# Optimization experiments

Hardware: AMD Instinct MI355X
Metric: run time of the kernel (lower is better)

The kernel has to match this reference:

```python
import jax, jax.numpy as jnp
import numpy as np

T = 16384       # tokens (flattened leading dims)
D_IN = 1024     # in_features
D_OUT = 1024    # out_features
E = 8           # n_models (experts)


def setup_inputs() -> dict:
    key = jax.random.key(0)
    kx, ki, kw, kb = jax.random.split(key, 4)
    x = jax.random.normal(kx, (T, D_IN), dtype=jnp.float32)
    idxs = jax.random.randint(ki, (T,), 0, E, dtype=jnp.int32)
    # Per-expert Linear params (nn.Linear default-ish init scale)
    scale = 1.0 / np.sqrt(D_IN)
    W = jax.random.uniform(kw, (E, D_IN, D_OUT), dtype=jnp.float32, minval=-scale, maxval=scale)
    b = jax.random.uniform(kb, (E, D_OUT), dtype=jnp.float32, minval=-scale, maxval=scale)
    return {"x": x, "idxs": idxs, "W": W, "b": b}


def reference(x, idxs, W, b):
    # Original: for each expert i, y[idxs==i] = Linear_i(x[idxs==i]); return relu(y).
    # Equivalent math: each token t gets expert idxs[t]'s linear.
    # Compute all experts densely (E is small), then gather the assigned row.
    ys = jnp.einsum('ti,eio->eto', x, W) + b[:, None, :]   # [E, T, D_OUT]
    y = ys[idxs, jnp.arange(x.shape[0])]                    # [T, D_OUT] pick assigned expert
    return jax.nn.relu(y)
```

## Files before the change

kernel.cpp:

```cpp
#include <hip/hip_runtime.h>
#include <hip/hip_bf16.h>
#include <stdint.h>


#define T_TOK 16384
#define DIN   1024
#define DOUT  1024
#define NE    8
#define BM    128
#define BN    128
#define BK    64
#define TPX   17
#define MAX_TILES 136
#define MP_MAX (T_TOK + NE * BM)

typedef __attribute__((ext_vector_type(8))) short short8;
typedef __attribute__((ext_vector_type(4))) short short4v;
typedef __attribute__((ext_vector_type(4))) float floatx4;
typedef __attribute__((ext_vector_type(4))) int int4v;

__device__ __forceinline__ short f2b(float f) {
  return __builtin_bit_cast(short, __float2bfloat16(f));
}
__device__ __forceinline__ float b2f(unsigned short u) {
  unsigned v = ((unsigned)u) << 16;
  return __builtin_bit_cast(float, v);
}
__device__ __forceinline__ void glds16(const void* g, void* l) {
  __builtin_amdgcn_global_load_lds(
      (__attribute__((address_space(1))) void*)g,
      (__attribute__((address_space(3))) void*)l, 16, 0, 0);
}

#define FLAG_OFF    0
#define NTILES_OFF  64
#define TABLE_OFF   1024
#define TPAD_OFF    8192
#define WT_OFF      81920
#define XB_OFF      16859136
#define WS_NEED     (16859136UL + (size_t)T_TOK * DIN * 2)

#define TRANS_BLOCKS 512
#define CONV_BLOCKS  1024

__global__ __launch_bounds__(1024) void k_front(
    const unsigned short* __restrict__ xu, const int* __restrict__ idxs,
    const void* __restrict__ Wsrc, short* __restrict__ Wt, short* __restrict__ xb,
    int* __restrict__ flag, int* __restrict__ ntiles,
    int4v* __restrict__ table, int* __restrict__ tpad) {
  __shared__ int fS;
  __shared__ unsigned short tile[128][130];
  __shared__ int wtot[16][NE], waveBase[16][NE];
  __shared__ int totS[NE], padS[NE + 1];

  int tid = threadIdx.x;
  if (tid == 0) fS = 0;
  __syncthreads();
  if (tid < 256) {
    int ex = (xu[tid] >> 7) & 0xFF;
    if (ex >= 0xC0) atomicOr(&fS, 1);
  }
  __syncthreads();
  int fp32 = fS;

  if (blockIdx.x >= 1 + TRANS_BLOCKS) {
    if (!fp32) return;
    int b2 = blockIdx.x - (1 + TRANS_BLOCKS);
    size_t base = ((size_t)b2 * 1024 + tid) * 16;
    const float* src = (const float*)xu + base;
    floatx4 a0 = *(const floatx4*)(src + 0);
    floatx4 a1 = *(const floatx4*)(src + 4);
    floatx4 a2 = *(const floatx4*)(src + 8);
    floatx4 a3 = *(const floatx4*)(src + 12);
    short8 o0, o1;
    #pragma unroll
    for (int j = 0; j < 4; ++j) {
      o0[j] = f2b(a0[j]); o0[4 + j] = f2b(a1[j]);
      o1[j] = f2b(a2[j]); o1[4 + j] = f2b(a3[j]);
    }
    *(short8*)(xb + base) = o0;
    *(short8*)(xb + base + 8) = o1;
    return;
  }

  if (blockIdx.x != 0) {
    int b = blockIdx.x - 1;
    int e = b >> 6, kt = (b >> 3) & 7, nt8 = b & 7;
    size_t ibase = (size_t)e * DIN * DOUT + (size_t)(kt * 128) * DOUT + nt8 * 128;
    int k = tid >> 3, n16 = (tid & 7) * 16;
    if (fp32) {
      const float* p = (const float*)Wsrc + ibase + (size_t)k * DOUT + n16;
      #pragma unroll
      for (int g = 0; g < 4; ++g) {
        floatx4 a = *(const floatx4*)(p + g * 4);
        #pragma unroll
        for (int j = 0; j < 4; ++j) tile[k][n16 + g * 4 + j] = (unsigned short)f2b(a[j]);
      }
    } else {
      const short* p = (const short*)Wsrc + ibase + (size_t)k * DOUT + n16;
      #pragma unroll
      for (int g = 0; g < 2; ++g) {
        short8 v = *(const short8*)(p + g * 8);
        #pragma unroll
        for (int j = 0; j < 8; ++j) tile[k][n16 + g * 8 + j] = (unsigned short)v[j];
      }
    }
    __syncthreads();
    int n = tid >> 3, k16 = (tid & 7) * 16;
    short8 o0, o1;
    #pragma unroll
    for (int j = 0; j < 8; ++j) {
      o0[j] = (short)tile[k16 + j][n];
      o1[j] = (short)tile[k16 + 8 + j][n];
    }
    size_t obase = (size_t)e * DOUT * DIN + (size_t)(nt8 * 128 + n) * DIN + kt * 128 + k16;
    *(short8*)(Wt + obase) = o0;
    *(short8*)(Wt + obase + 8) = o1;
    return;
  }

  int lane = tid & 63, w = tid >> 6;
  if (tid == 0) *flag = fp32;

  int c[NE];
  #pragma unroll
  for (int e = 0; e < NE; ++e) c[e] = 0;
  const int4v* iv = (const int4v*)idxs;
  int4v vv[4];
  #pragma unroll
  for (int it = 0; it < 4; ++it) {
    vv[it] = iv[tid * 4 + it];
    ++c[vv[it].x]; ++c[vv[it].y]; ++c[vv[it].z]; ++c[vv[it].w];
  }
  int incl[NE];
  #pragma unroll
  for (int e = 0; e < NE; ++e) {
    incl[e] = c[e];
    #pragma unroll
    for (int d = 1; d < 64; d <<= 1) {
      int o = __shfl_up(incl[e], d);
      if (lane >= d) incl[e] += o;
    }
  }
  if (lane == 63) {
    #pragma unroll
    for (int e = 0; e < NE; ++e) wtot[w][e] = incl[e];
  }
  __syncthreads();
  if (tid < NE) {
    int s = 0;
    for (int ww = 0; ww < 16; ++ww) s += wtot[ww][tid];
    totS[tid] = s;
  }
  __syncthreads();
  if (tid == 0) {
    int p = 0, tc = 0;
    for (int e = 0; e < NE; ++e) {
      padS[e] = p;
      int cn = totS[e];
      int nmt = (cn + BM - 1) >> 7;
      for (int m = 0; m < nmt; ++m) table[tc++] = (int4v){e, p + m * BM, 0, 0};
      p += nmt * BM;
    }
    padS[NE] = p;
    *ntiles = tc;
  }
  __syncthreads();
  if (tid < 128) {
    int ww = tid >> 3, e = tid & 7;
    int s = padS[e];
    for (int wp = 0; wp < ww; ++wp) s += wtot[wp][e];
    waveBase[ww][e] = s;
  }
  __syncthreads();
  int base[NE];
  #pragma unroll
  for (int e = 0; e < NE; ++e) base[e] = waveBase[w][e] + incl[e] - c[e];
  #pragma unroll
  for (int it = 0; it < 4; ++it) {
    #pragma unroll
    for (int cm = 0; cm < 4; ++cm) {
      int te = vv[it][cm];
      int tk = tid * 16 + it * 4 + cm;
      #pragma unroll
      for (int e0 = 0; e0 < NE; ++e0)
        if (te == e0) tpad[base[e0]++] = tk;
    }
  }
  #pragma unroll
  for (int e = 0; e < NE; ++e) {
    int start = padS[e] + totS[e];
    int len = padS[e + 1] - start;
    if (tid < len) tpad[start + tid] = -1;
  }
}

#define STAGE(bb, k0)                                                       \
  {                                                                         \
    _Pragma("unroll")                                                       \
    for (int s4 = 0; s4 < 4; ++s4)                                          \
      glds16(bG[s4] + (k0), (char*)lB[bb] + ldsOff[s4]);                    \
    _Pragma("unroll")                                                       \
    for (int s4 = 0; s4 < 4; ++s4)                                          \
      glds16(aG[s4] + (size_t)(k0) * 2, (char*)lA[bb] + ldsOff[s4]);        \
  }

__launch_bounds__(256, 2)
__global__ void k_gemm(const void* __restrict__ xv, const short* __restrict__ xb,
                       const void* __restrict__ bv,
                       const short* __restrict__ Wt, const int* __restrict__ tpad,
                       const int* __restrict__ ntilesp, const int4v* __restrict__ table,
                       const int* __restrict__ flagp, void* __restrict__ outv) {
  int bid = blockIdx.x;
  int xcd = bid & 7;
  int s = bid >> 3;
  int nt = s & 7;
  int ti = s >> 3;
  int t = xcd * TPX + ti;
  if (t >= *ntilesp) return;
  int4v te = table[t];
  int e = te.x, arow0 = te.y;
  int fp32 = *flagp;

  int tid = threadIdx.x;
  int lane = tid & 63;
  int wave = tid >> 6;

  __shared__ short lA[2][BM * BK];
  __shared__ short lB[2][BN * BK];
  __shared__ int tokS[BM];

  if (tid < BM) tokS[tid] = tpad[arow0 + tid];
  __syncthreads();

  const short* WtE = Wt + (size_t)e * DOUT * DIN + (size_t)(nt * BN) * DIN;
  const char* aBase = fp32 ? (const char*)xb : (const char*)xv;

  const char* aG[4];
  const short* bG[4];
  int ldsOff[4];
  #pragma unroll
  for (int s4 = 0; s4 < 4; ++s4) {
    int fl = tid + s4 * 256;
    int r = fl >> 3, p = fl & 7;
    int kc = p ^ (r & 7);
    int tok = tokS[r];
    if (tok < 0) tok = 0;
    aG[s4] = aBase + (size_t)tok * (DIN * 2) + kc * 16;
    bG[s4] = WtE + (size_t)r * DIN + kc * 8;
    ldsOff[s4] = (s4 * 256 + wave * 64) * 16;
  }

  int wm = wave & 1, wn = wave >> 1;
  int lrow = lane & 15, q = lane >> 4;
  int aOff[4][2], bOff[4][2];
  #pragma unroll
  for (int i = 0; i < 4; ++i) {
    int m = wm * 64 + i * 16 + lrow;
    #pragma unroll
    for (int h = 0; h < 2; ++h)
      aOff[i][h] = m * BK + (((h * 4 + q) ^ (m & 7)) * 8);
  }
  #pragma unroll
  for (int j = 0; j < 4; ++j) {
    int n = wn * 64 + j * 16 + lrow;
    #pragma unroll
    for (int h = 0; h < 2; ++h)
      bOff[j][h] = n * BK + (((h * 4 + q) ^ (n & 7)) * 8);
  }

  floatx4 acc[4][4];
  #pragma unroll
  for (int i = 0; i < 4; ++i)
    #pragma unroll
    for (int j = 0; j < 4; ++j)
      acc[i][j] = (floatx4){0.f, 0.f, 0.f, 0.f};

  STAGE(0, 0);
  asm volatile("s_waitcnt vmcnt(0)\n\ts_barrier" ::: "memory");

  int cur = 0;
  for (int kt = 0; kt < DIN / BK; ++kt) {
    if (kt < DIN / BK - 1) STAGE(cur ^ 1, (kt + 1) * BK);
    #pragma unroll
    for (int h = 0; h < 2; ++h) {
      short8 af[4], bf[4];
      #pragma unroll
      for (int i = 0; i < 4; ++i) af[i] = *(const short8*)(&lA[cur][0] + aOff[i][h]);
      #pragma unroll
      for (int j = 0; j < 4; ++j) bf[j] = *(const short8*)(&lB[cur][0] + bOff[j][h]);
      #pragma unroll
      for (int i = 0; i < 4; ++i)
        #pragma unroll
        for (int j = 0; j < 4; ++j)
          acc[i][j] = __builtin_amdgcn_mfma_f32_16x16x32_bf16(bf[j], af[i], acc[i][j], 0, 0, 0);
    }
    asm volatile("s_waitcnt vmcnt(0)\n\ts_barrier" ::: "memory");
    cur ^= 1;
  }

  #pragma unroll
  for (int i = 0; i < 4; ++i) {
    int tok = tokS[wm * 64 + i * 16 + lrow];
    if (tok < 0) continue;
    size_t rowb = (size_t)tok * DOUT + nt * BN + wn * 64 + q * 4;
    #pragma unroll
    for (int j = 0; j < 4; ++j) {
      int n = nt * BN + wn * 64 + j * 16 + q * 4;
      if (fp32) {
        floatx4 b4 = *(const floatx4*)((const float*)bv + e * DOUT + n);
        floatx4 o;
        #pragma unroll
        for (int r = 0; r < 4; ++r) {
          float v = acc[i][j][r] + b4[r];
          o[r] = v > 0.f ? v : 0.f;
        }
        *(floatx4*)((float*)outv + rowb + j * 16) = o;
      } else {
        short4v b4 = *(const short4v*)((const short*)bv + e * DOUT + n);
        short4v o;
        #pragma unroll
        for (int r = 0; r < 4; ++r) {
          float v = acc[i][j][r] + b2f((unsigned short)b4[r]);
          o[r] = f2b(v > 0.f ? v : 0.f);
        }
        *(short4v*)((short*)outv + rowb + j * 16) = o;
      }
    }
  }
}

__global__ void k_fallback(const void* __restrict__ xv, const int* __restrict__ idxs,
                           const void* __restrict__ Wv, const void* __restrict__ bv,
                           void* __restrict__ outv) {
  __shared__ float xrow[DIN];
  __shared__ int sflag;
  int t = blockIdx.x;
  int e = idxs[t];
  if (threadIdx.x == 0) {
    const unsigned short* u = (const unsigned short*)xv;
    int f = 0;
    for (int i = 0; i < 256; ++i) { int ex = (u[i] >> 7) & 0xFF; if (ex >= 0xC0) f = 1; }
    sflag = f;
  }
  __syncthreads();
  int fp32 = sflag;
  for (int i = threadIdx.x; i < DIN; i += 256)
    xrow[i] = fp32 ? ((const float*)xv)[(size_t)t * DIN + i]
                   : b2f(((const unsigned short*)xv)[(size_t)t * DIN + i]);
  __syncthreads();
  float a[4] = {0.f, 0.f, 0.f, 0.f};
  for (int k = 0; k < DIN; ++k) {
    float xk = xrow[k];
    size_t wb = (size_t)e * DIN * DOUT + (size_t)k * DOUT + threadIdx.x;
    #pragma unroll
    for (int j = 0; j < 4; ++j) {
      float w = fp32 ? ((const float*)Wv)[wb + j * 256]
                     : b2f(((const unsigned short*)Wv)[wb + j * 256]);
      a[j] += xk * w;
    }
  }
  #pragma unroll
  for (int j = 0; j < 4; ++j) {
    int n = threadIdx.x + j * 256;
    float bias = fp32 ? ((const float*)bv)[e * DOUT + n]
                      : b2f(((const unsigned short*)bv)[e * DOUT + n]);
    float v = a[j] + bias;
    v = v > 0.f ? v : 0.f;
    size_t o = (size_t)t * DOUT + n;
    if (fp32) ((float*)outv)[o] = v;
    else      ((short*)outv)[o] = f2b(v);
  }
}

extern "C" void kernel_launch(void* const* d_in, const int* in_sizes, int n_in,
                              void* d_out, int out_size, void* d_ws, size_t ws_size,
                              hipStream_t stream) {
  const void* x    = d_in[0];
  const int*  idxs = (const int*)d_in[1];
  const void* W    = d_in[2];
  const void* bias = d_in[3];

  if (ws_size < WS_NEED) {
    k_fallback<<<T_TOK, 256, 0, stream>>>(x, idxs, W, bias, d_out);
    return;
  }
  char* ws = (char*)d_ws;
  int* flag    = (int*)(ws + FLAG_OFF);
  int* ntiles  = (int*)(ws + NTILES_OFF);
  int4v* table = (int4v*)(ws + TABLE_OFF);
  int* tpad    = (int*)(ws + TPAD_OFF);
  short* Wt    = (short*)(ws + WT_OFF);
  short* xb    = (short*)(ws + XB_OFF);

  k_front<<<1 + TRANS_BLOCKS + CONV_BLOCKS, 1024, 0, stream>>>(
      (const unsigned short*)x, idxs, W, Wt, xb, flag, ntiles, table, tpad);
  k_gemm<<<8 * 8 * TPX, 256, 0, stream>>>(x, xb, bias, Wt, tpad, ntiles, table, flag, d_out);
}
```

Measured before the change: 222.8 us.

## Halve K tile to 32 to raise occupancy and unroll double-buffer steps

Shrinks the K tile from 64 to 32, which halves the LDS footprint per block. Launch bounds rise from 2 to 4 blocks per SIMD-group so more waves can hide latency. The swizzle is rewritten for 4-chunk rows, and the main loop is unrolled two steps at a time with constant buffer indices. The trade-off is twice as many barriers and waitcnt syncs per K sweep, and tighter register limits that may cause spills.

```diff
diff --git a/kernel.cpp b/kernel.cpp
--- a/kernel.cpp
+++ b/kernel.cpp
@@ -9,7 +9,7 @@
 #define NE    8
 #define BM    128
 #define BN    128
-#define BK    64
+#define BK    32
 #define TPX   17
 #define MAX_TILES 136
 #define MP_MAX (T_TOK + NE * BM)
@@ -195,17 +195,35 @@
   }
 }
 
-#define STAGE(bb, k0)                                                       \
+#define STAGE(NXT, k0)                                                      \
   {                                                                         \
     _Pragma("unroll")                                                       \
-    for (int s4 = 0; s4 < 4; ++s4)                                          \
-      glds16(bG[s4] + (k0), (char*)lB[bb] + ldsOff[s4]);                    \
-    _Pragma("unroll")                                                       \
-    for (int s4 = 0; s4 < 4; ++s4)                                          \
-      glds16(aG[s4] + (size_t)(k0) * 2, (char*)lA[bb] + ldsOff[s4]);        \
-  }
-
-__launch_bounds__(256, 2)
+    for (int s4 = 0; s4 < 2; ++s4)                                          \
+      glds16(bG[s4] + (k0), (char*)(lBbuf + (NXT) * (BN * BK)) + ldsOff[s4]); \
+    _Pragma("unroll")                                                       \
+    for (int s4 = 0; s4 < 2; ++s4)                                          \
+      glds16(aG[s4] + (size_t)(k0) * 2, (char*)(lAbuf + (NXT) * (BM * BK)) + ldsOff[s4]); \
+  }
+
+#define KSTEP(CUR, NXT, kNext, DO_STAGE)                                    \
+  {                                                                         \
+    if (DO_STAGE) STAGE(NXT, kNext);                                        \
+    short8 af[4], bf[4];                                                    \
+    _Pragma("unroll")                                                       \
+    for (int i = 0; i < 4; ++i)                                             \
+      af[i] = *(const short8*)(lAbuf + (CUR) * (BM * BK) + aOff[i]);        \
+    _Pragma("unroll")                                                       \
+    for (int j = 0; j < 4; ++j)                                             \
+      bf[j] = *(const short8*)(lBbuf + (CUR) * (BN * BK) + bOff[j]);        \
+    _Pragma("unroll")                                                       \
+    for (int i = 0; i < 4; ++i)                                             \
+      _Pragma("unroll")                                                     \
+      for (int j = 0; j < 4; ++j)                                           \
+        acc[i][j] = __builtin_amdgcn_mfma_f32_16x16x32_bf16(bf[j], af[i], acc[i][j], 0, 0, 0); \
+    asm volatile("s_waitcnt vmcnt(0)\n\ts_barrier" ::: "memory");           \
+  }
+
+__launch_bounds__(256, 4)
 __global__ void k_gemm(const void* __restrict__ xv, const short* __restrict__ xb,
                        const void* __restrict__ bv,
                        const short* __restrict__ Wt, const int* __restrict__ tpad,
@@ -226,8 +244,8 @@
   int lane = tid & 63;
   int wave = tid >> 6;
 
-  __shared__ short lA[2][BM * BK];
-  __shared__ short lB[2][BN * BK];
+  __shared__ short lAbuf[2 * BM * BK];
+  __shared__ short lBbuf[2 * BN * BK];
   __shared__ int tokS[BM];
 
   if (tid < BM) tokS[tid] = tpad[arow0 + tid];
@@ -236,14 +254,14 @@
   const short* WtE = Wt + (size_t)e * DOUT * DIN + (size_t)(nt * BN) * DIN;
   const char* aBase = fp32 ? (const char*)xb : (const char*)xv;
 
-  const char* aG[4];
-  const short* bG[4];
-  int ldsOff[4];
-  #pragma unroll
-  for (int s4 = 0; s4 < 4; ++s4) {
+  const char* aG[2];
+  const short* bG[2];
+  int ldsOff[2];
+  #pragma unroll
+  for (int s4 = 0; s4 < 2; ++s4) {
     int fl = tid + s4 * 256;
-    int r = fl >> 3, p = fl & 7;
-    int kc = p ^ (r & 7);
+    int r = fl >> 2, p = fl & 3;
+    int kc = p ^ ((r >> 1) & 3);
     int tok = tokS[r];
     if (tok < 0) tok = 0;
     aG[s4] = aBase + (size_t)tok * (DIN * 2) + kc * 16;
@@ -253,20 +271,16 @@
 
   int wm = wave & 1, wn = wave >> 1;
   int lrow = lane & 15, q = lane >> 4;
-  int aOff[4][2], bOff[4][2];
+  int aOff[4], bOff[4];
   #pragma unroll
   for (int i = 0; i < 4; ++i) {
     int m = wm * 64 + i * 16 + lrow;
-    #pragma unroll
-    for (int h = 0; h < 2; ++h)
-      aOff[i][h] = m * BK + (((h * 4 + q) ^ (m & 7)) * 8);
+    aOff[i] = m * BK + ((q ^ ((m >> 1) & 3)) * 8);
   }
   #pragma unroll
   for (int j = 0; j < 4; ++j) {
     int n = wn * 64 + j * 16 + lrow;
-    #pragma unroll
-    for (int h = 0; h < 2; ++h)
-      bOff[j][h] = n * BK + (((h * 4 + q) ^ (n & 7)) * 8);
+    bOff[j] = n * BK + ((q ^ ((n >> 1) & 3)) * 8);
   }
 
   floatx4 acc[4][4];
@@ -279,24 +293,9 @@
   STAGE(0, 0);
   asm volatile("s_waitcnt vmcnt(0)\n\ts_barrier" ::: "memory");
 
-  int cur = 0;
-  for (int kt = 0; kt < DIN / BK; ++kt) {
-    if (kt < DIN / BK - 1) STAGE(cur ^ 1, (kt + 1) * BK);
-    #pragma unroll
-    for (int h = 0; h < 2; ++h) {
-      short8 af[4], bf[4];
-      #pragma unroll
-      for (int i = 0; i < 4; ++i) af[i] = *(const short8*)(&lA[cur][0] + aOff[i][h]);
-      #pragma unroll
-      for (int j = 0; j < 4; ++j) bf[j] = *(const short8*)(&lB[cur][0] + bOff[j][h]);
-      #pragma unroll
-      for (int i = 0; i < 4; ++i)
-        #pragma unroll
-        for (int j = 0; j < 4; ++j)
-          acc[i][j] = __builtin_amdgcn_mfma_f32_16x16x32_bf16(bf[j], af[i], acc[i][j], 0, 0, 0);
-    }
-    asm volatile("s_waitcnt vmcnt(0)\n\ts_barrier" ::: "memory");
-    cur ^= 1;
+  for (int kt = 0; kt < DIN / BK; kt += 2) {
+    KSTEP(0, 1, (kt + 1) * BK, true);
+    KSTEP(1, 0, (kt + 2) * BK, (kt + 2) < DIN / BK);
   }
 
   #pragma unroll
```

Result: faster. 212.7 us (-4.5%).
